# Kernel tuning notes

Measured on AMD Instinct MI355X. Metric: run time of the kernel, lower is better.

Reference implementation:

```python
import jax, jax.numpy as jnp
import numpy as np

N = 100000   # nodes
E = 1600000  # edges (avg degree 16)
DIN, DH, DOUT = 128, 128, 64


def setup_inputs() -> dict:
    key = jax.random.key(0)
    ks = jax.random.split(key, 10)
    x = jax.random.normal(ks[0], (N, DIN), dtype=jnp.float32)
    edge_index = jax.random.randint(ks[1], (2, E), 0, N, dtype=jnp.int32)

    def kaiming(k, fan_out, fan_in):
        # kaiming_uniform_ with nonlinearity='relu': bound = sqrt(6/fan_in)
        bound = np.sqrt(6.0 / fan_in)
        return jax.random.uniform(k, (fan_out, fan_in), jnp.float32, -bound, bound)

    W1 = kaiming(ks[2], DH, DIN)
    W2 = kaiming(ks[3], DH, DH)
    W3 = kaiming(ks[4], DH, DH)
    W4 = kaiming(ks[5], DOUT, DH)
    b1 = jnp.zeros((DH,), jnp.float32)
    b2 = jnp.zeros((DH,), jnp.float32)
    b3 = jnp.zeros((DH,), jnp.float32)
    b4 = jnp.zeros((DOUT,), jnp.float32)
    return {"x": x, "edge_index": edge_index,
            "W1": W1, "b1": b1, "W2": W2, "b2": b2,
            "W3": W3, "b3": b3, "W4": W4, "b4": b4}


def reference(x, edge_index, W1, b1, W2, b2, W3, b3, W4, b4):
    n = x.shape[0]
    src, dst = edge_index[0], edge_index[1]
    # gcn_norm with add_self_loops=False: deg = in-degree at dst (unit weights)
    deg = jax.ops.segment_sum(jnp.ones(src.shape[0], x.dtype), dst, num_segments=n)
    deg_inv_sqrt = jnp.where(deg > 0, jax.lax.rsqrt(jnp.maximum(deg, 1.0)) * jnp.sqrt(jnp.maximum(deg, 1.0)) / jnp.maximum(deg, 1.0) * jnp.sqrt(jnp.maximum(deg, 1.0)), 0.0)
    deg_inv_sqrt = jnp.where(deg > 0, 1.0 / jnp.sqrt(jnp.maximum(deg, 1.0)), 0.0)
    norm = deg_inv_sqrt[src] * deg_inv_sqrt[dst]  # [E]

    def gcn_layer(h, W, b):
        h = h @ W.T                                # [n, out] dense transform
        msg = h[src] * norm[:, None]               # gather + scale  [E, out]
        out = jax.ops.segment_sum(msg, dst, num_segments=n)  # scatter-add
        return out + b

    h = jax.nn.relu(gcn_layer(x, W1, b1))
    h = jax.nn.relu(gcn_layer(h, W2, b2))
    h = jax.nn.relu(gcn_layer(h, W3, b3))
    return gcn_layer(h, W4, b4)
```

## Files before the change

### kernel.cpp

```cpp
#include <hip/hip_runtime.h>
#include <hip/hip_bf16.h>

#define CAP 64
#define SBCAP 12288

typedef __attribute__((ext_vector_type(8))) short bf16x8;
typedef __attribute__((ext_vector_type(4))) float f32x4;
typedef _Float16 f16;
typedef __attribute__((ext_vector_type(2))) _Float16 f16x2;
typedef __attribute__((ext_vector_type(8))) _Float16 f16x8;

__device__ __forceinline__ ushort f2bf(float f) {
    uint u = __float_as_uint(f);
    u = u + 0x7FFF + ((u >> 16) & 1);
    return (ushort)(u >> 16);
}
__device__ __forceinline__ float bf2f(ushort b) { return __uint_as_float(((uint)b) << 16); }

__device__ __forceinline__ int bkt(int d, int r) {
    int b = 0;
    if (d >= 4 * r) b = 4;
    if (d >= (b + 2) * r) b += 2;
    if (d >= (b + 1) * r) b += 1;
    return b;
}

__global__ __launch_bounds__(256) void route_kernel(const int* __restrict__ src,
                                                    const int* __restrict__ dst,
                                                    int E, int N,
                                                    uint* __restrict__ buf2,
                                                    int* __restrict__ gcur2, int NSUB) {
    __shared__ int lcnt[256], lbase[256];
    const int NS8 = 8 * NSUB;
    if (threadIdx.x < NS8) lcnt[threadIdx.x] = 0;
    __syncthreads();
    const int r = (N + 7) >> 3;
    const int e = (blockIdx.x * 256 + threadIdx.x) * 4;
    int sb_[4]; uint pk[4]; int ne = 0;
    if (e + 4 <= E) {
        int4 d4 = *(const int4*)(dst + e);
        int4 s4 = *(const int4*)(src + e);
        int ds_[4] = {d4.x, d4.y, d4.z, d4.w};
        int ss_[4] = {s4.x, s4.y, s4.z, s4.w};
#pragma unroll
        for (int k = 0; k < 4; ++k) {
            int b = bkt(ds_[k], r);
            int dl = ds_[k] - b * r;
            sb_[k] = b * NSUB + (dl >> 9);
            pk[k] = ((uint)ss_[k] << 14) | (uint)dl;
            atomicAdd(&lcnt[sb_[k]], 1);
        }
        ne = 4;
    } else {
        for (int t = e; t < E; ++t) {
            int b = bkt(dst[t], r);
            int dl = dst[t] - b * r;
            sb_[ne] = b * NSUB + (dl >> 9);
            pk[ne] = ((uint)src[t] << 14) | (uint)dl;
            atomicAdd(&lcnt[sb_[ne]], 1);
            ++ne;
        }
    }
    __syncthreads();
    if (threadIdx.x < NS8) {
        lbase[threadIdx.x] = atomicAdd(&gcur2[threadIdx.x], lcnt[threadIdx.x]);
        lcnt[threadIdx.x] = 0;
    }
    __syncthreads();
    for (int k = 0; k < ne; ++k) {
        int idx = lbase[sb_[k]] + atomicAdd(&lcnt[sb_[k]], 1);
        if (idx < SBCAP) buf2[(size_t)sb_[k] * SBCAP + idx] = pk[k];
    }
}

__global__ __launch_bounds__(256) void fillsort_kernel(const uint* __restrict__ buf2,
                                                       const int* __restrict__ gcur2,
                                                       int* __restrict__ fil,
                                                       int* __restrict__ csr, int N, int NSUB) {
    __shared__ uint stage[SBCAP];
    __shared__ int lcnt[512];
    const int xg = blockIdx.x & 7;
    const int sub = blockIdx.x >> 3;
    const int sb = xg * NSUB + sub;
    const int r = (N + 7) >> 3;
    const int lo_dl = sub << 9;
    const int ndst = min(512, r - lo_dl);
    if (ndst <= 0) return;
    int cnt = gcur2[sb];
    if (cnt > SBCAP) cnt = SBCAP;
    for (int i = threadIdx.x; i < cnt; i += 256) stage[i] = buf2[(size_t)sb * SBCAP + i];
    for (int i = threadIdx.x; i < ndst; i += 256) lcnt[i] = 0;
    __syncthreads();
    const int lo_d = xg * r + lo_dl;
    for (int i = threadIdx.x; i < cnt; i += 256) {
        uint pk = stage[i];
        int dll = (int)(pk & 0x3FFFu) - lo_dl;
        int s = (int)(pk >> 14);
        int p = atomicAdd(&lcnt[dll], 1);
        if (p < CAP) csr[(size_t)(lo_d + dll) * CAP + p] = s;
    }
    __syncthreads();
    for (int i = threadIdx.x; i < ndst; i += 256) {
        int d = lo_d + i;
        if (d < N) fil[d] = lcnt[i];
    }
}

__global__ void prep_kernel(const float* __restrict__ W1, const float* __restrict__ W2,
                            const float* __restrict__ W3, const float* __restrict__ W4,
                            ushort* __restrict__ hilo,
                            const int* __restrict__ cnt, float* __restrict__ dis, int N) {
    int blk = blockIdx.x;
    if (blk < 224) {
        int i = blk * 256 + threadIdx.x;
        const float* W;
        ushort* hi;
        int off;
        if (i < 16384)      { W = W1; hi = hilo;          off = i; }
        else if (i < 32768) { W = W2; hi = hilo + 32768;  off = i - 16384; }
        else if (i < 49152) { W = W3; hi = hilo + 65536;  off = i - 32768; }
        else                { W = W4; hi = hilo + 98304;  off = i - 49152; }
        float w = W[off];
        ushort h = f2bf(w);
        int span = (i < 49152) ? 16384 : 8192;
        hi[off] = h;
        hi[off + span] = f2bf(w - bf2f(h));
    } else {
        int i = (blk - 224) * 256 + threadIdx.x;
        if (i < N) {
            int c = cnt[i];
            dis[i] = (c > 0) ? rsqrtf((float)c) : 0.0f;
        }
    }
}

__global__ __launch_bounds__(256) void xprep_kernel(const float* __restrict__ x,
                                                    const int* __restrict__ cnt,
                                                    f16* __restrict__ h0, int N) {
    int q = blockIdx.x * 256 + threadIdx.x;
    if (q * 4 >= N * 128) return;
    int row = q >> 5;
    int c = cnt[row];
    float dd = (c > 0) ? rsqrtf((float)c) : 0.0f;
    float4 v = *(const float4*)(x + (size_t)q * 4);
    f16 o[4] = {(f16)(v.x * dd), (f16)(v.y * dd), (f16)(v.z * dd), (f16)(v.w * dd)};
    *(f16x2*)(h0 + (size_t)q * 4) = (f16x2){o[0], o[1]};
    *(f16x2*)(h0 + (size_t)q * 4 + 2) = (f16x2){o[2], o[3]};
}

template <bool DO_RELU>
__global__ __launch_bounds__(256) void fused_kernel(const f16* __restrict__ hin,
                                                    const ushort* __restrict__ Whi,
                                                    const ushort* __restrict__ Wlo,
                                                    const int* __restrict__ csr,
                                                    const int* __restrict__ cnt,
                                                    const float* __restrict__ dis,
                                                    const float* __restrict__ bias,
                                                    f16* __restrict__ hout, int N) {
    __shared__ float a[32][132];
    const int wave = threadIdx.x >> 6;
    const int lane = threadIdx.x & 63;
    const int nb8 = gridDim.x >> 3;
    const int vblk = (blockIdx.x & 7) * nb8 + (blockIdx.x >> 3);
    const int rowBase = vblk * 32;

    for (int k = 0; k < 8; ++k) {
        const int nl = wave * 8 + k;
        const int node = rowBase + nl;
        float acc0 = 0.f, acc1 = 0.f;
        if (node < N) {
            int c = cnt[node];
            if (c > CAP) c = CAP;
            const int* lst = csr + (size_t)node * CAP;
            int j = 0;
            for (; j + 8 <= c; j += 8) {
                int4 sA = *(const int4*)(lst + j);
                int4 sB = *(const int4*)(lst + j + 4);
                f16x2 t0 = *(const f16x2*)(hin + (size_t)sA.x * 128 + lane * 2);
                f16x2 t1 = *(const f16x2*)(hin + (size_t)sA.y * 128 + lane * 2);
                f16x2 t2 = *(const f16x2*)(hin + (size_t)sA.z * 128 + lane * 2);
                f16x2 t3 = *(const f16x2*)(hin + (size_t)sA.w * 128 + lane * 2);
                f16x2 t4 = *(const f16x2*)(hin + (size_t)sB.x * 128 + lane * 2);
                f16x2 t5 = *(const f16x2*)(hin + (size_t)sB.y * 128 + lane * 2);
                f16x2 t6 = *(const f16x2*)(hin + (size_t)sB.z * 128 + lane * 2);
                f16x2 t7 = *(const f16x2*)(hin + (size_t)sB.w * 128 + lane * 2);
                acc0 += (((float)t0[0] + (float)t1[0]) + ((float)t2[0] + (float)t3[0])) +
                        (((float)t4[0] + (float)t5[0]) + ((float)t6[0] + (float)t7[0]));
                acc1 += (((float)t0[1] + (float)t1[1]) + ((float)t2[1] + (float)t3[1])) +
                        (((float)t4[1] + (float)t5[1]) + ((float)t6[1] + (float)t7[1]));
            }
            for (; j + 4 <= c; j += 4) {
                int4 sA = *(const int4*)(lst + j);
                f16x2 t0 = *(const f16x2*)(hin + (size_t)sA.x * 128 + lane * 2);
                f16x2 t1 = *(const f16x2*)(hin + (size_t)sA.y * 128 + lane * 2);
                f16x2 t2 = *(const f16x2*)(hin + (size_t)sA.z * 128 + lane * 2);
                f16x2 t3 = *(const f16x2*)(hin + (size_t)sA.w * 128 + lane * 2);
                acc0 += ((float)t0[0] + (float)t1[0]) + ((float)t2[0] + (float)t3[0]);
                acc1 += ((float)t0[1] + (float)t1[1]) + ((float)t2[1] + (float)t3[1]);
            }
            for (; j < c; ++j) {
                int s = lst[j];
                f16x2 t = *(const f16x2*)(hin + (size_t)s * 128 + lane * 2);
                acc0 += (float)t[0];
                acc1 += (float)t[1];
            }
            float dd = dis[node];
            acc0 *= dd;
            acc1 *= dd;
        }
        *(float2*)(&a[nl][lane * 2]) = make_float2(acc0, acc1);
    }
    __syncthreads();

    const int lr = lane & 15;
    const int kg = lane >> 4;
    const int rt = wave & 1;
    const int ctb = (wave >> 1) * 4;
    f32x4 acc[4];
#pragma unroll
    for (int c = 0; c < 4; ++c) acc[c] = (f32x4){0.f, 0.f, 0.f, 0.f};

#pragma unroll
    for (int kt = 0; kt < 4; ++kt) {
        float f[8];
#pragma unroll
        for (int j = 0; j < 8; ++j) f[j] = a[rt * 16 + lr][kt * 32 + kg * 8 + j];
        bf16x8 Ah, Al;
#pragma unroll
        for (int j = 0; j < 8; ++j) {
            ushort hb = f2bf(f[j]);
            Ah[j] = (short)hb;
            Al[j] = (short)f2bf(f[j] - bf2f(hb));
        }
#pragma unroll
        for (int c = 0; c < 4; ++c) {
            const size_t wo = (size_t)((ctb + c) * 16 + lr) * 128 + kt * 32 + kg * 8;
            bf16x8 Bh = *(const bf16x8*)(Whi + wo);
            bf16x8 Bl = *(const bf16x8*)(Wlo + wo);
            acc[c] = __builtin_amdgcn_mfma_f32_16x16x32_bf16(Al, Bh, acc[c], 0, 0, 0);
            acc[c] = __builtin_amdgcn_mfma_f32_16x16x32_bf16(Ah, Bl, acc[c], 0, 0, 0);
            acc[c] = __builtin_amdgcn_mfma_f32_16x16x32_bf16(Ah, Bh, acc[c], 0, 0, 0);
        }
    }

#pragma unroll
    for (int j = 0; j < 4; ++j) {
        int row = rowBase + rt * 16 + kg * 4 + j;
        if (row < N) {
            float dd = dis[row];
#pragma unroll
            for (int c = 0; c < 4; ++c) {
                int col = (ctb + c) * 16 + lr;
                float v = acc[c][j] + bias[col];
                if (DO_RELU) v = fmaxf(v, 0.f);
                hout[(size_t)row * 128 + col] = (f16)(v * dd);
            }
        }
    }
}

__global__ __launch_bounds__(256) void gemm64_kernel(const f16* __restrict__ F,
                                                     const ushort* __restrict__ Whi,
                                                     const ushort* __restrict__ Wlo,
                                                     f16* __restrict__ G, int N) {
    constexpr int CT = 4;
    const int wave = threadIdx.x >> 6;
    const int lane = threadIdx.x & 63;
    const int lr = lane & 15;
    const int kg = lane >> 4;
    const int rowBase = blockIdx.x * 128 + wave * 32;

    f32x4 acc[2][CT];
#pragma unroll
    for (int rt = 0; rt < 2; ++rt)
#pragma unroll
        for (int c = 0; c < CT; ++c) acc[rt][c] = (f32x4){0.f, 0.f, 0.f, 0.f};

#pragma unroll
    for (int kt = 0; kt < 4; ++kt) {
        bf16x8 Ah[2], Al[2];
#pragma unroll
        for (int rt = 0; rt < 2; ++rt) {
            int row = rowBase + rt * 16 + lr;
            row = row < N ? row : N - 1;
            f16x8 v = *(const f16x8*)(F + (size_t)row * 128 + kt * 32 + kg * 8);
            bf16x8 h, l;
#pragma unroll
            for (int j = 0; j < 8; ++j) {
                float fv = (float)v[j];
                ushort hb = f2bf(fv);
                h[j] = (short)hb;
                l[j] = (short)f2bf(fv - bf2f(hb));
            }
            Ah[rt] = h;
            Al[rt] = l;
        }
#pragma unroll
        for (int c = 0; c < CT; ++c) {
            const size_t wo = (size_t)(c * 16 + lr) * 128 + kt * 32 + kg * 8;
            bf16x8 Bh = *(const bf16x8*)(Whi + wo);
            bf16x8 Bl = *(const bf16x8*)(Wlo + wo);
#pragma unroll
            for (int rt = 0; rt < 2; ++rt) {
                acc[rt][c] = __builtin_amdgcn_mfma_f32_16x16x32_bf16(Al[rt], Bh, acc[rt][c], 0, 0, 0);
                acc[rt][c] = __builtin_amdgcn_mfma_f32_16x16x32_bf16(Ah[rt], Bl, acc[rt][c], 0, 0, 0);
                acc[rt][c] = __builtin_amdgcn_mfma_f32_16x16x32_bf16(Ah[rt], Bh, acc[rt][c], 0, 0, 0);
            }
        }
    }
#pragma unroll
    for (int rt = 0; rt < 2; ++rt)
#pragma unroll
        for (int j = 0; j < 4; ++j) {
            int row = rowBase + rt * 16 + kg * 4 + j;
            if (row < N)
#pragma unroll
                for (int c = 0; c < CT; ++c)
                    G[(size_t)row * 64 + c * 16 + lr] = (f16)acc[rt][c][j];
        }
}

__global__ __launch_bounds__(256) void agg64_kernel(const f16* __restrict__ g,
                                                    const int* __restrict__ csr,
                                                    const int* __restrict__ cnt,
                                                    const float* __restrict__ dis,
                                                    const float* __restrict__ bias,
                                                    float* __restrict__ out, int N) {
    const int nb8 = gridDim.x >> 3;
    const int vblk = (blockIdx.x & 7) * nb8 + (blockIdx.x >> 3);
    int node = vblk * 4 + (threadIdx.x >> 6);
    if (node >= N) return;
    int lane = threadIdx.x & 63;

    int c = cnt[node];
    if (c > CAP) c = CAP;
    const int* lst = csr + (size_t)node * CAP;
    float acc0 = 0.f;

    int j = 0;
    for (; j + 8 <= c; j += 8) {
        int4 sA = *(const int4*)(lst + j);
        int4 sB = *(const int4*)(lst + j + 4);
        float u0 = (float)g[(size_t)sA.x * 64 + lane];
        float u1 = (float)g[(size_t)sA.y * 64 + lane];
        float u2 = (float)g[(size_t)sA.z * 64 + lane];
        float u3 = (float)g[(size_t)sA.w * 64 + lane];
        float u4 = (float)g[(size_t)sB.x * 64 + lane];
        float u5 = (float)g[(size_t)sB.y * 64 + lane];
        float u6 = (float)g[(size_t)sB.z * 64 + lane];
        float u7 = (float)g[(size_t)sB.w * 64 + lane];
        acc0 += ((u0 + u1) + (u2 + u3)) + ((u4 + u5) + (u6 + u7));
    }
    for (; j + 4 <= c; j += 4) {
        int4 sA = *(const int4*)(lst + j);
        float u0 = (float)g[(size_t)sA.x * 64 + lane];
        float u1 = (float)g[(size_t)sA.y * 64 + lane];
        float u2 = (float)g[(size_t)sA.z * 64 + lane];
        float u3 = (float)g[(size_t)sA.w * 64 + lane];
        acc0 += (u0 + u1) + (u2 + u3);
    }
    for (; j < c; ++j) acc0 += (float)g[(size_t)lst[j] * 64 + lane];

    float v0 = fmaf(dis[node], acc0, bias[lane]);
    out[(size_t)node * 64 + lane] = v0;
}

extern "C" void kernel_launch(void* const* d_in, const int* in_sizes, int n_in,
                              void* d_out, int out_size, void* d_ws, size_t ws_size,
                              hipStream_t stream) {
    const float* x  = (const float*)d_in[0];
    const int*   ei = (const int*)d_in[1];
    const float* W1 = (const float*)d_in[2];
    const float* b1 = (const float*)d_in[3];
    const float* W2 = (const float*)d_in[4];
    const float* b2 = (const float*)d_in[5];
    const float* W3 = (const float*)d_in[6];
    const float* b3 = (const float*)d_in[7];
    const float* W4 = (const float*)d_in[8];
    const float* b4 = (const float*)d_in[9];

    const int N = in_sizes[0] / 128;
    const int E = in_sizes[1] / 2;
    const int* src = ei;
    const int* dst = ei + E;
    const int r = (N + 7) >> 3;
    const int NSUB = (r + 511) >> 9;
    const int NS8 = 8 * NSUB;

    char* w = (char*)d_ws;
    f16*   H0  = (f16*)w;   w += (size_t)N * 128 * 2;
    f16*   H1  = (f16*)w;   w += (size_t)N * 128 * 2;
    int*   csr = (int*)w;   w += (size_t)N * CAP * 4;
    float* dis = (float*)w; w += (size_t)N * 4;
    int*   fil = (int*)w;   w += (size_t)N * 4;
    int*   gcur2 = (int*)w; w += (size_t)NS8 * 4;
    ushort* Whl = (ushort*)w; w += (16384 * 6 + 8192 * 2) * 2;
    ushort* Whi1 = Whl;          ushort* Wlo1 = Whl + 16384;
    ushort* Whi2 = Whl + 32768;  ushort* Wlo2 = Whl + 49152;
    ushort* Whi3 = Whl + 65536;  ushort* Wlo3 = Whl + 81920;
    ushort* Whi4 = Whl + 98304;  ushort* Wlo4 = Whl + 106496;
    uint* buf2 = (uint*)H1;
    f16*  G4   = H0;

    float* out = (float*)d_out;

    hipMemsetAsync(fil, 0, ((size_t)N + NS8) * sizeof(int), stream);

    route_kernel<<<((E + 3) / 4 + 255) / 256, 256, 0, stream>>>(src, dst, E, N, buf2, gcur2, NSUB);
    fillsort_kernel<<<8 * NSUB, 256, 0, stream>>>(buf2, gcur2, fil, csr, N, NSUB);
    prep_kernel<<<224 + (N + 255) / 256, 256, 0, stream>>>(W1, W2, W3, W4, Whl, fil, dis, N);
    xprep_kernel<<<((N * 128 / 4) + 255) / 256, 256, 0, stream>>>(x, fil, H0, N);

    const int fgrid = (((N + 31) / 32 + 7) / 8) * 8;
    const int agrid = (((N + 3) / 4 + 7) / 8) * 8;

    fused_kernel<true><<<fgrid, 256, 0, stream>>>(H0, Whi1, Wlo1, csr, fil, dis, b1, H1, N);
    fused_kernel<true><<<fgrid, 256, 0, stream>>>(H1, Whi2, Wlo2, csr, fil, dis, b2, H0, N);
    fused_kernel<true><<<fgrid, 256, 0, stream>>>(H0, Whi3, Wlo3, csr, fil, dis, b3, H1, N);
    gemm64_kernel<<<(N + 127) / 128, 256, 0, stream>>>(H1, Whi4, Wlo4, G4, N);
    agg64_kernel<<<agrid, 256, 0, stream>>>(G4, csr, fil, dis, b4, out, N);
}
```

Measured before the change: 624.8 us.

## Process nodes in degree-sorted order to balance per-block gather work

Builds a per-XCD-group degree histogram in fillsort, then scans it and scatters node ids into a degree-sorted permutation. Each fused layer kernel now takes its 32 rows per block from this permutation, so nodes in a block have similar neighbour counts and waves diverge less. Padding slots point at a valid node, which removes the bounds checks; those duplicates recompute and rewrite identical rows. The cost is three extra small launches, an extra indirection on perm, and scattered rather than contiguous output-row writes.

```diff
diff --git a/kernel.cpp b/kernel.cpp
--- a/kernel.cpp
+++ b/kernel.cpp
@@ -76,7 +76,9 @@
 __global__ __launch_bounds__(256) void fillsort_kernel(const uint* __restrict__ buf2,
                                                        const int* __restrict__ gcur2,
                                                        int* __restrict__ fil,
-                                                       int* __restrict__ csr, int N, int NSUB) {
+                                                       int* __restrict__ csr,
+                                                       int* __restrict__ bins,
+                                                       int N, int NSUB) {
     __shared__ uint stage[SBCAP];
     __shared__ int lcnt[512];
     const int xg = blockIdx.x & 7;
@@ -102,7 +104,38 @@
     __syncthreads();
     for (int i = threadIdx.x; i < ndst; i += 256) {
         int d = lo_d + i;
-        if (d < N) fil[d] = lcnt[i];
+        if (d < N) {
+            fil[d] = lcnt[i];
+            atomicAdd(&bins[xg * 64 + min(lcnt[i], 63)], 1);
+        }
+    }
+}
+
+__global__ void scan_kernel(const int* __restrict__ bins, int* __restrict__ gbase, int S) {
+    int w = threadIdx.x >> 6, l = threadIdx.x & 63, d = 63 - l;
+    int v = bins[w * 64 + d];
+    int s = v;
+#pragma unroll
+    for (int off = 1; off < 64; off <<= 1) {
+        int t = __shfl_up(s, off, 64);
+        if (l >= off) s += t;
+    }
+    gbase[w * 64 + d] = w * S + (s - v);
+}
+
+__global__ void initperm_kernel(int* __restrict__ perm, int S, int r) {
+    int s = blockIdx.x * 256 + threadIdx.x;
+    if (s < 8 * S) perm[s] = (s / S) * r;
+}
+
+__global__ void scatter_kernel(const int* __restrict__ fil, int* __restrict__ gbase,
+                               int* __restrict__ perm, int N, int r) {
+    int i = blockIdx.x * 256 + threadIdx.x;
+    if (i < N) {
+        int xg = bkt(i, r);
+        int d = min(fil[i], 63);
+        int pos = atomicAdd(&gbase[xg * 64 + d], 1);
+        perm[pos] = i;
     }
 }
 
@@ -156,59 +189,54 @@
                                                     const int* __restrict__ cnt,
                                                     const float* __restrict__ dis,
                                                     const float* __restrict__ bias,
-                                                    f16* __restrict__ hout, int N) {
+                                                    const int* __restrict__ perm,
+                                                    f16* __restrict__ hout, int S) {
     __shared__ float a[32][132];
     const int wave = threadIdx.x >> 6;
     const int lane = threadIdx.x & 63;
-    const int nb8 = gridDim.x >> 3;
-    const int vblk = (blockIdx.x & 7) * nb8 + (blockIdx.x >> 3);
-    const int rowBase = vblk * 32;
+    const int pbase = (blockIdx.x & 7) * S + (blockIdx.x >> 3) * 32;
 
     for (int k = 0; k < 8; ++k) {
         const int nl = wave * 8 + k;
-        const int node = rowBase + nl;
+        const int node = perm[pbase + nl];
         float acc0 = 0.f, acc1 = 0.f;
-        if (node < N) {
-            int c = cnt[node];
-            if (c > CAP) c = CAP;
-            const int* lst = csr + (size_t)node * CAP;
-            int j = 0;
-            for (; j + 8 <= c; j += 8) {
-                int4 sA = *(const int4*)(lst + j);
-                int4 sB = *(const int4*)(lst + j + 4);
-                f16x2 t0 = *(const f16x2*)(hin + (size_t)sA.x * 128 + lane * 2);
-                f16x2 t1 = *(const f16x2*)(hin + (size_t)sA.y * 128 + lane * 2);
-                f16x2 t2 = *(const f16x2*)(hin + (size_t)sA.z * 128 + lane * 2);
-                f16x2 t3 = *(const f16x2*)(hin + (size_t)sA.w * 128 + lane * 2);
-                f16x2 t4 = *(const f16x2*)(hin + (size_t)sB.x * 128 + lane * 2);
-                f16x2 t5 = *(const f16x2*)(hin + (size_t)sB.y * 128 + lane * 2);
-                f16x2 t6 = *(const f16x2*)(hin + (size_t)sB.z * 128 + lane * 2);
-                f16x2 t7 = *(const f16x2*)(hin + (size_t)sB.w * 128 + lane * 2);
-                acc0 += (((float)t0[0] + (float)t1[0]) + ((float)t2[0] + (float)t3[0])) +
-                        (((float)t4[0] + (float)t5[0]) + ((float)t6[0] + (float)t7[0]));
-                acc1 += (((float)t0[1] + (float)t1[1]) + ((float)t2[1] + (float)t3[1])) +
-                        (((float)t4[1] + (float)t5[1]) + ((float)t6[1] + (float)t7[1]));
-            }
-            for (; j + 4 <= c; j += 4) {
-                int4 sA = *(const int4*)(lst + j);
-                f16x2 t0 = *(const f16x2*)(hin + (size_t)sA.x * 128 + lane * 2);
-                f16x2 t1 = *(const f16x2*)(hin + (size_t)sA.y * 128 + lane * 2);
-                f16x2 t2 = *(const f16x2*)(hin + (size_t)sA.z * 128 + lane * 2);
-                f16x2 t3 = *(const f16x2*)(hin + (size_t)sA.w * 128 + lane * 2);
-                acc0 += ((float)t0[0] + (float)t1[0]) + ((float)t2[0] + (float)t3[0]);
-                acc1 += ((float)t0[1] + (float)t1[1]) + ((float)t2[1] + (float)t3[1]);
-            }
-            for (; j < c; ++j) {
-                int s = lst[j];
-                f16x2 t = *(const f16x2*)(hin + (size_t)s * 128 + lane * 2);
-                acc0 += (float)t[0];
-                acc1 += (float)t[1];
-            }
-            float dd = dis[node];
-            acc0 *= dd;
-            acc1 *= dd;
-        }
-        *(float2*)(&a[nl][lane * 2]) = make_float2(acc0, acc1);
+        int c = cnt[node];
+        if (c > CAP) c = CAP;
+        const int* lst = csr + (size_t)node * CAP;
+        int j = 0;
+        for (; j + 8 <= c; j += 8) {
+            int4 sA = *(const int4*)(lst + j);
+            int4 sB = *(const int4*)(lst + j + 4);
+            f16x2 t0 = *(const f16x2*)(hin + (size_t)sA.x * 128 + lane * 2);
+            f16x2 t1 = *(const f16x2*)(hin + (size_t)sA.y * 128 + lane * 2);
+            f16x2 t2 = *(const f16x2*)(hin + (size_t)sA.z * 128 + lane * 2);
+            f16x2 t3 = *(const f16x2*)(hin + (size_t)sA.w * 128 + lane * 2);
+            f16x2 t4 = *(const f16x2*)(hin + (size_t)sB.x * 128 + lane * 2);
+            f16x2 t5 = *(const f16x2*)(hin + (size_t)sB.y * 128 + lane * 2);
+            f16x2 t6 = *(const f16x2*)(hin + (size_t)sB.z * 128 + lane * 2);
+            f16x2 t7 = *(const f16x2*)(hin + (size_t)sB.w * 128 + lane * 2);
+            acc0 += (((float)t0[0] + (float)t1[0]) + ((float)t2[0] + (float)t3[0])) +
+                    (((float)t4[0] + (float)t5[0]) + ((float)t6[0] + (float)t7[0]));
+            acc1 += (((float)t0[1] + (float)t1[1]) + ((float)t2[1] + (float)t3[1])) +
+                    (((float)t4[1] + (float)t5[1]) + ((float)t6[1] + (float)t7[1]));
+        }
+        for (; j + 4 <= c; j += 4) {
+            int4 sA = *(const int4*)(lst + j);
+            f16x2 t0 = *(const f16x2*)(hin + (size_t)sA.x * 128 + lane * 2);
+            f16x2 t1 = *(const f16x2*)(hin + (size_t)sA.y * 128 + lane * 2);
+            f16x2 t2 = *(const f16x2*)(hin + (size_t)sA.z * 128 + lane * 2);
+            f16x2 t3 = *(const f16x2*)(hin + (size_t)sA.w * 128 + lane * 2);
+            acc0 += ((float)t0[0] + (float)t1[0]) + ((float)t2[0] + (float)t3[0]);
+            acc1 += ((float)t0[1] + (float)t1[1]) + ((float)t2[1] + (float)t3[1]);
+        }
+        for (; j < c; ++j) {
+            int s = lst[j];
+            f16x2 t = *(const f16x2*)(hin + (size_t)s * 128 + lane * 2);
+            acc0 += (float)t[0];
+            acc1 += (float)t[1];
+        }
+        float dd = dis[node];
+        *(float2*)(&a[nl][lane * 2]) = make_float2(acc0 * dd, acc1 * dd);
     }
     __syncthreads();
 
@@ -245,16 +273,14 @@
 
 #pragma unroll
     for (int j = 0; j < 4; ++j) {
-        int row = rowBase + rt * 16 + kg * 4 + j;
-        if (row < N) {
-            float dd = dis[row];
-#pragma unroll
-            for (int c = 0; c < 4; ++c) {
-                int col = (ctb + c) * 16 + lr;
-                float v = acc[c][j] + bias[col];
-                if (DO_RELU) v = fmaxf(v, 0.f);
-                hout[(size_t)row * 128 + col] = (f16)(v * dd);
-            }
+        int node = perm[pbase + rt * 16 + kg * 4 + j];
+        float dd = dis[node];
+#pragma unroll
+        for (int c = 0; c < 4; ++c) {
+            int col = (ctb + c) * 16 + lr;
+            float v = acc[c][j] + bias[col];
+            if (DO_RELU) v = fmaxf(v, 0.f);
+            hout[(size_t)node * 128 + col] = (f16)(v * dd);
         }
     }
 }
@@ -387,6 +413,11 @@
     const int NSUB = (r + 511) >> 9;
     const int NS8 = 8 * NSUB;
 
+    const int nrows32 = (N + 31) / 32;
+    const int nb8 = (nrows32 + 7) / 8;
+    const int fgrid = nb8 * 8;
+    const int S = nb8 * 32;
+
     char* w = (char*)d_ws;
     f16*   H0  = (f16*)w;   w += (size_t)N * 128 * 2;
     f16*   H1  = (f16*)w;   w += (size_t)N * 128 * 2;
@@ -394,6 +425,9 @@
     float* dis = (float*)w; w += (size_t)N * 4;
     int*   fil = (int*)w;   w += (size_t)N * 4;
     int*   gcur2 = (int*)w; w += (size_t)NS8 * 4;
+    int*   bins = (int*)w;  w += 512 * 4;
+    int*   gbase = (int*)w; w += 512 * 4;
+    int*   perm = (int*)w;  w += (size_t)8 * S * 4;
     ushort* Whl = (ushort*)w; w += (16384 * 6 + 8192 * 2) * 2;
     ushort* Whi1 = Whl;          ushort* Wlo1 = Whl + 16384;
     ushort* Whi2 = Whl + 32768;  ushort* Wlo2 = Whl + 49152;
@@ -404,19 +438,21 @@
 
     float* out = (float*)d_out;
 
-    hipMemsetAsync(fil, 0, ((size_t)N + NS8) * sizeof(int), stream);
+    hipMemsetAsync(fil, 0, ((size_t)N + NS8 + 512) * sizeof(int), stream);
 
     route_kernel<<<((E + 3) / 4 + 255) / 256, 256, 0, stream>>>(src, dst, E, N, buf2, gcur2, NSUB);
-    fillsort_kernel<<<8 * NSUB, 256, 0, stream>>>(buf2, gcur2, fil, csr, N, NSUB);
+    fillsort_kernel<<<8 * NSUB, 256, 0, stream>>>(buf2, gcur2, fil, csr, bins, N, NSUB);
     prep_kernel<<<224 + (N + 255) / 256, 256, 0, stream>>>(W1, W2, W3, W4, Whl, fil, dis, N);
+    scan_kernel<<<1, 512, 0, stream>>>(bins, gbase, S);
+    initperm_kernel<<<(8 * S + 255) / 256, 256, 0, stream>>>(perm, S, r);
+    scatter_kernel<<<(N + 255) / 256, 256, 0, stream>>>(fil, gbase, perm, N, r);
     xprep_kernel<<<((N * 128 / 4) + 255) / 256, 256, 0, stream>>>(x, fil, H0, N);
 
-    const int fgrid = (((N + 31) / 32 + 7) / 8) * 8;
     const int agrid = (((N + 3) / 4 + 7) / 8) * 8;
 
-    fused_kernel<true><<<fgrid, 256, 0, stream>>>(H0, Whi1, Wlo1, csr, fil, dis, b1, H1, N);
-    fused_kernel<true><<<fgrid, 256, 0, stream>>>(H1, Whi2, Wlo2, csr, fil, dis, b2, H0, N);
-    fused_kernel<true><<<fgrid, 256, 0, stream>>>(H0, Whi3, Wlo3, csr, fil, dis, b3, H1, N);
+    fused_kernel<true><<<fgrid, 256, 0, stream>>>(H0, Whi1, Wlo1, csr, fil, dis, b1, perm, H1, S);
+    fused_kernel<true><<<fgrid, 256, 0, stream>>>(H1, Whi2, Wlo2, csr, fil, dis, b2, perm, H0, S);
+    fused_kernel<true><<<fgrid, 256, 0, stream>>>(H0, Whi3, Wlo3, csr, fil, dis, b3, perm, H1, S);
     gemm64_kernel<<<(N + 127) / 128, 256, 0, stream>>>(H1, Whi4, Wlo4, G4, N);
     agg64_kernel<<<agrid, 256, 0, stream>>>(G4, csr, fil, dis, b4, out, N);
 }
```

Result: slower. 684.2 us (+9.5%).
